# Kernel optimization log

Hardware: AMD Instinct MI355X
Metric: run time of the kernel (lower is better)

The kernel has to match this reference:

```python
import jax, jax.numpy as jnp
import numpy as np

# --- reconstructed config / key constants (from init_kwargs) ---
SCALES = (8, 16, 32)                      # patch sizes tiling H, W
TEMPORAL_WINDOWS = (0, 250, 500, 750, 1000)
KEY_INT = 0x5D1CE5                        # deterministic int derived from watermark_key+model_id
BASE_STRENGTH = 0.05
HASH_MOD = 10007
TWO_PI = 6.2831853


def _watermark_bias_map(latent, timestep):
    """Vectorized equivalent of the per-scale / per-patch Python loops.

    For each scale p: tile HxW into (H/p)x(W/p) patches, pool latent over
    (batch, channel, patch) -> scalar per patch, combine with a keyed integer
    hash phase into g in [-1,1], scale by a per-(scale,timestep) strength, and
    paint the constant bias over each patch region (the spatial mask).
    Returns a [H, W] bias map broadcastable over [B, C, H, W].
    """
    B, C, H, W = latent.shape
    # temporal bucket (timestep is a static Python int)
    bucket = int(np.searchsorted(np.asarray(TEMPORAL_WINDOWS), timestep, side='right') - 1)
    total = jnp.zeros((H, W), dtype=latent.dtype)
    for p in SCALES:
        gh, gw = H // p, W // p
        # pooled features per patch: mean over batch, channels, and patch pixels -> [gh, gw]
        pooled = latent.reshape(B, C, gh, p, gw, p).mean(axis=(0, 1, 3, 5))
        # keyed hash phase per patch (top-left coords i*p, j*p)
        base = (KEY_INT * 2654435761 + p * 97 + bucket * 139) % HASH_MOD
        i = (jnp.arange(gh, dtype=jnp.int32) * (p * 131))[:, None]
        j = (jnp.arange(gw, dtype=jnp.int32) * (p * 137))[None, :]
        h = (base + i + j) % HASH_MOD                           # [gh, gw] int
        phase = h.astype(latent.dtype) * (TWO_PI / HASH_MOD)
        g = jnp.cos(pooled * 3.0 + phase)                       # g_value in [-1, 1]
        strength = np.float32(BASE_STRENGTH / np.sqrt(p) * np.exp(-timestep / 1000.0))
        # broadcast patch-constant bias over the full spatial mask region
        total = total + jnp.repeat(jnp.repeat(g * strength, p, axis=0), p, axis=1)
    return total


def setup_inputs() -> dict:
    key = jax.random.key(0)
    k1, k2 = jax.random.split(key)
    B, C, H, W = 64, 4, 256, 256
    noise = jax.random.normal(k1, (B, C, H, W), dtype=jnp.float32)
    latent = jax.random.normal(k2, (B, C, H, W), dtype=jnp.float32)
    return {"noise": noise, "latent": latent, "timestep": 500}


def reference(noise, latent, timestep):
    bias = _watermark_bias_map(latent, timestep)        # [H, W]
    return noise + bias[None, None, :, :]               # [B, C, H, W]
```

## Files before the change

kernel.cpp:

```cpp
#include <hip/hip_runtime.h>
#include <hip/hip_bf16.h>

static constexpr unsigned long long KEY_MUL =
    (6102245ULL * 2654435761ULL) % 10007ULL;
static constexpr int HASH_MOD = 10007;

template <int NCH>
__global__ __launch_bounds__(256) void pool_kernel(
    const float* __restrict__ latent, float* __restrict__ ws_partial) {
  constexpr int PPC = 256 / NCH;
  const int pr = blockIdx.y;
  const int ch = blockIdx.x;
  const int t  = threadIdx.x;
  const int cl = t & 63;
  const int rg = t >> 6;

  float acc = 0.0f;
  const float4* base = reinterpret_cast<const float4*>(latent);
#pragma unroll 8
  for (int pl = 0; pl < PPC; ++pl) {
    const float4* prow = base + (size_t)(ch * PPC + pl) * 16384;
#pragma unroll
    for (int rr = 0; rr < 2; ++rr) {
      float4 v = prow[(pr * 8 + rg + rr * 4) * 64 + cl];
      acc += (v.x + v.y) + (v.z + v.w);
    }
  }
  acc += __shfl_xor(acc, 1, 64);

  __shared__ float lds[4][32];
  if ((cl & 1) == 0) lds[rg][cl >> 1] = acc;
  __syncthreads();
  if (t < 32) {
    float s = (lds[0][t] + lds[1][t]) + (lds[2][t] + lds[3][t]);
    ws_partial[(pr * 32 + t) * NCH + ch] = s;
  }
}

template <int NCH>
__global__ __launch_bounds__(256, 4) void bias_add_kernel(
    const float* __restrict__ noise, const float* __restrict__ ws_partial,
    const int* __restrict__ tstep, float* __restrict__ out) {
  const int t = threadIdx.x;
  const int b = blockIdx.x;
  const int q = b & 3;
  const int lr = t >> 5;
  const int lc = t & 31;

  __shared__ float s8[256];
  __shared__ float btot[256];

  const int ts = *tstep;

  {
    const int patch = (8 * q + lr) * 32 + lc;
    float s = 0.0f;
    if constexpr (NCH >= 4) {
      const float4* p4 =
          reinterpret_cast<const float4*>(ws_partial) + patch * (NCH / 4);
#pragma unroll
      for (int c = 0; c < NCH / 4; ++c) {
        float4 v = p4[c];
        s += (v.x + v.y) + (v.z + v.w);
      }
    } else {
#pragma unroll
      for (int c = 0; c < NCH; ++c) s += ws_partial[patch * NCH + c];
    }
    s8[t] = s;
  }
  __syncthreads();

  {
    int bucket = -1;
    const int wins[5] = {0, 250, 500, 750, 1000};
#pragma unroll
    for (int k = 0; k < 5; ++k) bucket += (ts >= wins[k]) ? 1 : 0;

    const double expo = exp(-(double)ts / 1000.0);
    const float phase_k = (float)(6.2831853 / 10007.0);

    float bias = 0.0f;
    {
      const int p = 8, i = 8 * q + lr, j = lc;
      const long long bb =
          ((long long)KEY_MUL + p * 97 + bucket * 139 + 10 * HASH_MOD) % HASH_MOD;
      const int h = (int)((bb + (long long)i * (p * 131) + (long long)j * (p * 137)) % HASH_MOD);
      const float pooled = s8[t] * (1.0f / 16384.0f);
      const float strength = (float)(0.05 / sqrt(8.0) * expo);
      bias += cosf(pooled * 3.0f + (float)h * phase_k) * strength;
    }
    {
      const int p = 16, i = 4 * q + (lr >> 1), j = lc >> 1;
      const long long bb =
          ((long long)KEY_MUL + p * 97 + bucket * 139 + 10 * HASH_MOD) % HASH_MOD;
      const int h = (int)((bb + (long long)i * (p * 131) + (long long)j * (p * 137)) % HASH_MOD);
      const int r0 = (lr & ~1) * 32, c0 = lc & ~1;
      const float s = (s8[r0 + c0] + s8[r0 + c0 + 1]) +
                      (s8[r0 + 32 + c0] + s8[r0 + 32 + c0 + 1]);
      const float pooled = s * (1.0f / 65536.0f);
      const float strength = (float)(0.05 / sqrt(16.0) * expo);
      bias += cosf(pooled * 3.0f + (float)h * phase_k) * strength;
    }
    {
      const int p = 32, i = 2 * q + (lr >> 2), j = lc >> 2;
      const long long bb =
          ((long long)KEY_MUL + p * 97 + bucket * 139 + 10 * HASH_MOD) % HASH_MOD;
      const int h = (int)((bb + (long long)i * (p * 131) + (long long)j * (p * 137)) % HASH_MOD);
      const int r0 = (lr & ~3) * 32, c0 = lc & ~3;
      float s = 0.0f;
#pragma unroll
      for (int di = 0; di < 4; ++di)
#pragma unroll
        for (int dj = 0; dj < 4; ++dj) s += s8[r0 + di * 32 + c0 + dj];
      const float pooled = s * (1.0f / 262144.0f);
      const float strength = (float)(0.05 / sqrt(32.0) * expo);
      bias += cosf(pooled * 3.0f + (float)h * phase_k) * strength;
    }
    btot[t] = bias;
  }
  __syncthreads();

  {
    const size_t slab = (size_t)(b >> 2) * 16384 + (size_t)q * 4096;
    const float4* __restrict__ n4 = reinterpret_cast<const float4*>(noise) + slab;
    float4* __restrict__ o4 = reinterpret_cast<float4*>(out) + slab;
    const int c8 = (t & 63) >> 1;
    const int r0 = t >> 6;
#pragma unroll
    for (int kk = 0; kk < 4; ++kk) {
      float4 v[4];
      float bs[4];
#pragma unroll
      for (int k2 = 0; k2 < 4; ++k2) {
        const int k = kk * 4 + k2;
        v[k2] = n4[k * 256 + t];
        const int lrow = k * 4 + r0;
        bs[k2] = btot[(lrow >> 3) * 32 + c8];
      }
#pragma unroll
      for (int k2 = 0; k2 < 4; ++k2) {
        const int k = kk * 4 + k2;
        float4 w = v[k2];
        w.x += bs[k2]; w.y += bs[k2]; w.z += bs[k2]; w.w += bs[k2];
        o4[k * 256 + t] = w;
      }
    }
  }
}

extern "C" void kernel_launch(void* const* d_in, const int* in_sizes, int n_in,
                              void* d_out, int out_size, void* d_ws, size_t ws_size,
                              hipStream_t stream) {
  const float* noise  = (const float*)d_in[0];
  const float* latent = (const float*)d_in[1];
  const int*   tstep  = (const int*)d_in[2];
  float* out = (float*)d_out;
  float* ws  = (float*)d_ws;

  const size_t need32 = (size_t)(1024 * 32) * sizeof(float);
  const size_t need8  = (size_t)(1024 * 8) * sizeof(float);

  if (ws_size >= need32) {
    pool_kernel<32><<<dim3(32, 32), 256, 0, stream>>>(latent, ws);
    bias_add_kernel<32><<<1024, 256, 0, stream>>>(noise, ws, tstep, out);
  } else if (ws_size >= need8) {
    pool_kernel<8><<<dim3(8, 32), 256, 0, stream>>>(latent, ws);
    bias_add_kernel<8><<<1024, 256, 0, stream>>>(noise, ws, tstep, out);
  } else {
    pool_kernel<1><<<dim3(1, 32), 256, 0, stream>>>(latent, ws);
    bias_add_kernel<1><<<1024, 256, 0, stream>>>(noise, ws, tstep, out);
  }
}
```

Baseline: 38.14 us.

## Split pool and bias-add work into smaller blocks with batched loads and nontemporal stores

Adds a dedicated 32-channel pool kernel that splits each patch row into two half-blocks and issues all eight float4 loads up front. It also halves the bias-add tile to four patch rows per block, which doubles the grid. In the bias-add kernel, the hash and strength maths move from double/int64 to float/int, and all noise loads are issued before the adds. Output uses nontemporal stores. The goal is more memory-level parallelism and occupancy on a bandwidth-bound op, at the cost of redundant per-block bias computation and only 128 active threads during the bias phase.

Result: no change. 38.88 us (+1.9%).

```diff
diff --git a/kernel.cpp b/kernel.cpp
--- a/kernel.cpp
+++ b/kernel.cpp
@@ -1,20 +1,48 @@
 #include <hip/hip_runtime.h>
 #include <hip/hip_bf16.h>
 
-static constexpr unsigned long long KEY_MUL =
-    (6102245ULL * 2654435761ULL) % 10007ULL;
+static constexpr int KEY_MUL =
+    (int)((6102245ULL * 2654435761ULL) % 10007ULL);
 static constexpr int HASH_MOD = 10007;
 
+typedef float f32x4 __attribute__((ext_vector_type(4)));
+
+__global__ __launch_bounds__(256, 8) void pool_kernel32(
+    const float* __restrict__ latent, float* __restrict__ ws_partial) {
+  const int ch = blockIdx.x;
+  const int pr = blockIdx.y >> 1;
+  const int half = blockIdx.y & 1;
+  const int t = threadIdx.x;
+  const int cl = t & 31;
+  const int rg = t >> 5;
+
+  const float4* base = reinterpret_cast<const float4*>(latent);
+  float4 v[8];
+#pragma unroll
+  for (int pl = 0; pl < 8; ++pl)
+    v[pl] = base[(size_t)(ch * 8 + pl) * 16384 + (pr * 8 + rg) * 64 +
+                 half * 32 + cl];
+  float acc = 0.0f;
+#pragma unroll
+  for (int pl = 0; pl < 8; ++pl) acc += (v[pl].x + v[pl].y) + (v[pl].z + v[pl].w);
+  acc += __shfl_xor(acc, 1, 64);
+
+  __shared__ float lds[8][16];
+  if ((cl & 1) == 0) lds[rg][cl >> 1] = acc;
+  __syncthreads();
+  if (t < 16) {
+    float s = ((lds[0][t] + lds[1][t]) + (lds[2][t] + lds[3][t])) +
+              ((lds[4][t] + lds[5][t]) + (lds[6][t] + lds[7][t]));
+    ws_partial[(pr * 32 + half * 16 + t) * 32 + ch] = s;
+  }
+}
+
 template <int NCH>
-__global__ __launch_bounds__(256) void pool_kernel(
+__global__ __launch_bounds__(256) void pool_kernel_legacy(
     const float* __restrict__ latent, float* __restrict__ ws_partial) {
   constexpr int PPC = 256 / NCH;
-  const int pr = blockIdx.y;
-  const int ch = blockIdx.x;
-  const int t  = threadIdx.x;
-  const int cl = t & 63;
-  const int rg = t >> 6;
-
+  const int pr = blockIdx.y, ch = blockIdx.x, t = threadIdx.x;
+  const int cl = t & 63, rg = t >> 6;
   float acc = 0.0f;
   const float4* base = reinterpret_cast<const float4*>(latent);
 #pragma unroll 8
@@ -27,7 +55,6 @@
     }
   }
   acc += __shfl_xor(acc, 1, 64);
-
   __shared__ float lds[4][32];
   if ((cl & 1) == 0) lds[rg][cl >> 1] = acc;
   __syncthreads();
@@ -38,22 +65,22 @@
 }
 
 template <int NCH>
-__global__ __launch_bounds__(256, 4) void bias_add_kernel(
+__global__ __launch_bounds__(256, 8) void bias_add_kernel(
     const float* __restrict__ noise, const float* __restrict__ ws_partial,
     const int* __restrict__ tstep, float* __restrict__ out) {
   const int t = threadIdx.x;
   const int b = blockIdx.x;
-  const int q = b & 3;
-  const int lr = t >> 5;
-  const int lc = t & 31;
+  const int q = b & 7;
 
-  __shared__ float s8[256];
-  __shared__ float btot[256];
+  __shared__ float s8[128];
+  __shared__ float btot[128];
 
   const int ts = *tstep;
 
-  {
-    const int patch = (8 * q + lr) * 32 + lc;
+  if (t < 128) {
+    const int lr = t >> 5;
+    const int lc = t & 31;
+    const int patch = (4 * q + lr) * 32 + lc;
     float s = 0.0f;
     if constexpr (NCH >= 4) {
       const float4* p4 =
@@ -71,80 +98,77 @@
   }
   __syncthreads();
 
-  {
+  if (t < 128) {
+    const int lr = t >> 5;
+    const int lc = t & 31;
+    const int pr = 4 * q + lr;
+
     int bucket = -1;
     const int wins[5] = {0, 250, 500, 750, 1000};
 #pragma unroll
     for (int k = 0; k < 5; ++k) bucket += (ts >= wins[k]) ? 1 : 0;
 
-    const double expo = exp(-(double)ts / 1000.0);
+    const float expo = expf((float)(-ts) * 0.001f);
     const float phase_k = (float)(6.2831853 / 10007.0);
 
     float bias = 0.0f;
     {
-      const int p = 8, i = 8 * q + lr, j = lc;
-      const long long bb =
-          ((long long)KEY_MUL + p * 97 + bucket * 139 + 10 * HASH_MOD) % HASH_MOD;
-      const int h = (int)((bb + (long long)i * (p * 131) + (long long)j * (p * 137)) % HASH_MOD);
+      const int bb = (KEY_MUL + 8 * 97 + bucket * 139) % HASH_MOD;
+      const int h = (bb + pr * (8 * 131) + lc * (8 * 137)) % HASH_MOD;
       const float pooled = s8[t] * (1.0f / 16384.0f);
-      const float strength = (float)(0.05 / sqrt(8.0) * expo);
-      bias += cosf(pooled * 3.0f + (float)h * phase_k) * strength;
+      bias += cosf(pooled * 3.0f + (float)h * phase_k) *
+              (0.0176776695296637f * expo);
     }
     {
-      const int p = 16, i = 4 * q + (lr >> 1), j = lc >> 1;
-      const long long bb =
-          ((long long)KEY_MUL + p * 97 + bucket * 139 + 10 * HASH_MOD) % HASH_MOD;
-      const int h = (int)((bb + (long long)i * (p * 131) + (long long)j * (p * 137)) % HASH_MOD);
+      const int bb = (KEY_MUL + 16 * 97 + bucket * 139) % HASH_MOD;
+      const int h =
+          (bb + (pr >> 1) * (16 * 131) + (lc >> 1) * (16 * 137)) % HASH_MOD;
       const int r0 = (lr & ~1) * 32, c0 = lc & ~1;
       const float s = (s8[r0 + c0] + s8[r0 + c0 + 1]) +
                       (s8[r0 + 32 + c0] + s8[r0 + 32 + c0 + 1]);
       const float pooled = s * (1.0f / 65536.0f);
-      const float strength = (float)(0.05 / sqrt(16.0) * expo);
-      bias += cosf(pooled * 3.0f + (float)h * phase_k) * strength;
+      bias += cosf(pooled * 3.0f + (float)h * phase_k) *
+              (0.0125f * expo);
     }
     {
-      const int p = 32, i = 2 * q + (lr >> 2), j = lc >> 2;
-      const long long bb =
-          ((long long)KEY_MUL + p * 97 + bucket * 139 + 10 * HASH_MOD) % HASH_MOD;
-      const int h = (int)((bb + (long long)i * (p * 131) + (long long)j * (p * 137)) % HASH_MOD);
-      const int r0 = (lr & ~3) * 32, c0 = lc & ~3;
+      const int bb = (KEY_MUL + 32 * 97 + bucket * 139) % HASH_MOD;
+      const int h = (bb + q * (32 * 131) + (lc >> 2) * (32 * 137)) % HASH_MOD;
+      const int c0 = lc & ~3;
       float s = 0.0f;
 #pragma unroll
       for (int di = 0; di < 4; ++di)
 #pragma unroll
-        for (int dj = 0; dj < 4; ++dj) s += s8[r0 + di * 32 + c0 + dj];
+        for (int dj = 0; dj < 4; ++dj) s += s8[di * 32 + c0 + dj];
       const float pooled = s * (1.0f / 262144.0f);
-      const float strength = (float)(0.05 / sqrt(32.0) * expo);
-      bias += cosf(pooled * 3.0f + (float)h * phase_k) * strength;
+      bias += cosf(pooled * 3.0f + (float)h * phase_k) *
+              (0.00883883476483184f * expo);
     }
     btot[t] = bias;
   }
   __syncthreads();
 
   {
-    const size_t slab = (size_t)(b >> 2) * 16384 + (size_t)q * 4096;
-    const float4* __restrict__ n4 = reinterpret_cast<const float4*>(noise) + slab;
-    float4* __restrict__ o4 = reinterpret_cast<float4*>(out) + slab;
+    const size_t slab = (size_t)(b >> 3) * 16384 + (size_t)q * 2048;
+    const f32x4* __restrict__ n4 = reinterpret_cast<const f32x4*>(noise) + slab;
+    f32x4* __restrict__ o4 = reinterpret_cast<f32x4*>(out) + slab;
     const int c8 = (t & 63) >> 1;
     const int r0 = t >> 6;
+
+    f32x4 v[8];
 #pragma unroll
-    for (int kk = 0; kk < 4; ++kk) {
-      float4 v[4];
-      float bs[4];
+    for (int k = 0; k < 8; ++k) v[k] = n4[k * 256 + t];
+
+    float bs[8];
 #pragma unroll
-      for (int k2 = 0; k2 < 4; ++k2) {
-        const int k = kk * 4 + k2;
-        v[k2] = n4[k * 256 + t];
-        const int lrow = k * 4 + r0;
-        bs[k2] = btot[(lrow >> 3) * 32 + c8];
-      }
+    for (int k = 0; k < 8; ++k) {
+      const int lrow = k * 4 + r0;
+      bs[k] = btot[(lrow >> 3) * 32 + c8];
+    }
 #pragma unroll
-      for (int k2 = 0; k2 < 4; ++k2) {
-        const int k = kk * 4 + k2;
-        float4 w = v[k2];
-        w.x += bs[k2]; w.y += bs[k2]; w.z += bs[k2]; w.w += bs[k2];
-        o4[k * 256 + t] = w;
-      }
+    for (int k = 0; k < 8; ++k) {
+      f32x4 w = v[k];
+      w.x += bs[k]; w.y += bs[k]; w.z += bs[k]; w.w += bs[k];
+      __builtin_nontemporal_store(w, &o4[k * 256 + t]);
     }
   }
 }
@@ -162,13 +186,13 @@
   const size_t need8  = (size_t)(1024 * 8) * sizeof(float);
 
   if (ws_size >= need32) {
-    pool_kernel<32><<<dim3(32, 32), 256, 0, stream>>>(latent, ws);
-    bias_add_kernel<32><<<1024, 256, 0, stream>>>(noise, ws, tstep, out);
+    pool_kernel32<<<dim3(32, 64), 256, 0, stream>>>(latent, ws);
+    bias_add_kernel<32><<<2048, 256, 0, stream>>>(noise, ws, tstep, out);
   } else if (ws_size >= need8) {
-    pool_kernel<8><<<dim3(8, 32), 256, 0, stream>>>(latent, ws);
-    bias_add_kernel<8><<<1024, 256, 0, stream>>>(noise, ws, tstep, out);
+    pool_kernel_legacy<8><<<dim3(8, 32), 256, 0, stream>>>(latent, ws);
+    bias_add_kernel<8><<<2048, 256, 0, stream>>>(noise, ws, tstep, out);
   } else {
-    pool_kernel<1><<<dim3(1, 32), 256, 0, stream>>>(latent, ws);
-    bias_add_kernel<1><<<1024, 256, 0, stream>>>(noise, ws, tstep, out);
+    pool_kernel_legacy<1><<<dim3(1, 32), 256, 0, stream>>>(latent, ws);
+    bias_add_kernel<1><<<2048, 256, 0, stream>>>(noise, ws, tstep, out);
   }
 }
```
